# Optimization experiments

Hardware: AMD Instinct MI355X
Metric: run time of the kernel (lower is better)

Reference implementation:

```python
import jax, jax.numpy as jnp
import numpy as np

N, D_IN = 8192, 256
L1_DIMS = [256, 128, 64]   # linear_list1
GNN_DIMS = [64, 64]        # gnn_list
L2_DIMS = [64, 32]         # linear_list2


def leaky(x):
    return jnp.where(x >= 0, x, 0.1 * x)


def _lin_params(key, din, dout, scale=0.05):
    k1, k2 = jax.random.split(key)
    W = jax.random.normal(k1, (dout, din), dtype=jnp.float32) * scale
    b = jax.random.normal(k2, (dout,), dtype=jnp.float32) * scale
    return W, b


def setup_inputs() -> dict:
    key = jax.random.key(0)
    ks = jax.random.split(key, 8)
    x = jax.random.normal(ks[0], (N, D_IN), dtype=jnp.float32)
    A = jax.random.uniform(ks[1], (N, N), dtype=jnp.float32)
    W1_0, b1_0 = _lin_params(ks[2], L1_DIMS[0], L1_DIMS[1])
    W1_1, b1_1 = _lin_params(ks[3], L1_DIMS[1], L1_DIMS[2])
    a = jax.random.normal(ks[4], (L1_DIMS[-1],), dtype=jnp.float32)
    Wg_0, bg_0 = _lin_params(ks[5], GNN_DIMS[0], GNN_DIMS[1])
    W2_0, b2_0 = _lin_params(ks[6], L2_DIMS[0], L2_DIMS[1])
    return {"x": x, "A": A, "W1_0": W1_0, "b1_0": b1_0, "W1_1": W1_1,
            "b1_1": b1_1, "a": a, "Wg_0": Wg_0, "bg_0": bg_0,
            "W2_0": W2_0, "b2_0": b2_0}


def reference(x, A, W1_0, b1_0, W1_1, b1_1, a, Wg_0, bg_0, W2_0, b2_0):
    # MLP encoder (linear_list1) with leakyrelu(0.1)
    x = leaky(x @ W1_0.T + b1_0)
    x = leaky(x @ W1_1.T + b1_1)  # [N, 64]

    # GAT-style scores: (x_i - x_j) @ a == s_i - s_j with s = x @ a
    s = x @ a                               # [N]
    S = jnp.exp(leaky(s[:, None] - s[None, :])) * A  # [N, N]
    S = S / jnp.sum(S, axis=-1, keepdims=True)

    # L1 = mean_ij( mean_d (x_i - x_j)^2 * S_ij )
    D = x.shape[-1]
    sq = jnp.sum(x * x, axis=-1) / D        # [N]
    pair_mse = sq[:, None] + sq[None, :] - (2.0 / D) * (x @ x.T)  # [N, N]
    L1 = jnp.mean(pair_mse * S)
    L2 = jnp.mean(S * S)

    # GNN layer(s): x = leakyrelu(Linear(S @ x))
    x = leaky((S @ x) @ Wg_0.T + bg_0)

    # output head (linear_list2), no activation
    x = x @ W2_0.T + b2_0
    return (x, L1, L2)
```

## Files before the change

kernel.cpp:

```cpp
#include <hip/hip_runtime.h>
#include <cstddef>

#define NROWS 8192
#define RA_STR 72

typedef __attribute__((ext_vector_type(8))) short bf16x8;
typedef __attribute__((ext_vector_type(4))) short short4v;
typedef __attribute__((ext_vector_type(4))) float f32x4;

__device__ __forceinline__ short f2bf(float f) {
  unsigned u = __float_as_uint(f);
  u += 0x7fffu + ((u >> 16) & 1u);
  return (short)(u >> 16);
}
__device__ __forceinline__ float leaky_f(float v) { return v >= 0.0f ? v : 0.1f * v; }

extern "C" __global__ void __launch_bounds__(256)
encoder_kernel(const float* __restrict__ x, const float* __restrict__ W10,
               const float* __restrict__ b10, const float* __restrict__ W11,
               const float* __restrict__ b11, const float* __restrict__ avec,
               float* __restrict__ x2, float* __restrict__ sarr,
               float* __restrict__ sqarr, short* __restrict__ x2bfT) {
  __shared__ float xr[4][256];
  __shared__ float h1[4][128];
  const int t = threadIdx.x;
  const int r0 = blockIdx.x * 4;
#pragma unroll
  for (int r = 0; r < 4; ++r) xr[r][t] = x[(size_t)(r0 + r) * 256 + t];
  __syncthreads();
  if (t < 128) {
    float acc[4];
    const float b = b10[t];
#pragma unroll
    for (int r = 0; r < 4; ++r) acc[r] = b;
    const float* wrow = W10 + t * 256;
    for (int c = 0; c < 256; c += 4) {
      const float4 wv = *(const float4*)(wrow + c);
#pragma unroll
      for (int r = 0; r < 4; ++r) {
        acc[r] = fmaf(wv.x, xr[r][c], acc[r]);
        acc[r] = fmaf(wv.y, xr[r][c + 1], acc[r]);
        acc[r] = fmaf(wv.z, xr[r][c + 2], acc[r]);
        acc[r] = fmaf(wv.w, xr[r][c + 3], acc[r]);
      }
    }
#pragma unroll
    for (int r = 0; r < 4; ++r) h1[r][t] = leaky_f(acc[r]);
  }
  __syncthreads();
  if (t < 64) {
    float acc[4];
    const float b = b11[t];
#pragma unroll
    for (int r = 0; r < 4; ++r) acc[r] = b;
    const float* wrow = W11 + t * 128;
    for (int c = 0; c < 128; c += 4) {
      const float4 wv = *(const float4*)(wrow + c);
#pragma unroll
      for (int r = 0; r < 4; ++r) {
        acc[r] = fmaf(wv.x, h1[r][c], acc[r]);
        acc[r] = fmaf(wv.y, h1[r][c + 1], acc[r]);
        acc[r] = fmaf(wv.z, h1[r][c + 2], acc[r]);
        acc[r] = fmaf(wv.w, h1[r][c + 3], acc[r]);
      }
    }
    const float av = avec[t];
#pragma unroll
    for (int r = 0; r < 4; ++r) {
      const float v = leaky_f(acc[r]);
      x2[(size_t)(r0 + r) * 64 + t] = v;
      x2bfT[(size_t)t * NROWS + r0 + r] = f2bf(v);
      float ps = v * av, pq = v * v;
#pragma unroll
      for (int off = 1; off < 64; off <<= 1) {
        ps += __shfl_xor(ps, off);
        pq += __shfl_xor(pq, off);
      }
      if (t == 0) { sarr[r0 + r] = ps; sqarr[r0 + r] = pq * (1.0f / 64.0f); }
    }
  }
}

extern "C" __global__ void __launch_bounds__(256)
fused_attn_kernel(const float* __restrict__ A, const float* __restrict__ sarr,
                  const float* __restrict__ sqarr, const short* __restrict__ x2bfT,
                  float* __restrict__ yp, float* __restrict__ rsp,
                  float* __restrict__ ssp, float* __restrict__ wsp) {
  __shared__ short rawA[64 * RA_STR];
  __shared__ short xbT[64 * RA_STR];
  __shared__ float sj[64];
  __shared__ float sqj[64];

  const int t = threadIdx.x;
  const int bi = blockIdx.x & 127;
  const int js = blockIdx.x >> 7;
  const int i0 = bi * 64;
  const int jbase = js * 2048;
  const int lane = t & 63;
  const int w = t >> 6;

  const int lrb = t >> 4;
  const int lc = (t & 15) * 4;

  float si[4];
#pragma unroll
  for (int p = 0; p < 4; ++p) si[p] = sarr[i0 + lrb + 16 * p];

  float prsum[4] = {0.f, 0.f, 0.f, 0.f};
  float psumsq[4] = {0.f, 0.f, 0.f, 0.f};
  float pwsq[4] = {0.f, 0.f, 0.f, 0.f};

  const int m0 = (w >> 1) * 32;
  const int n0 = (w & 1) * 32;
  const int fr = lane & 15;
  const int fk = (lane >> 4) * 8;

  f32x4 acc[2][2];
#pragma unroll
  for (int fm = 0; fm < 2; ++fm)
#pragma unroll
    for (int fn = 0; fn < 2; ++fn)
      acc[fm][fn] = (f32x4){0.f, 0.f, 0.f, 0.f};

  float4 areg[4];
#pragma unroll
  for (int p = 0; p < 4; ++p)
    areg[p] = *(const float4*)(A + (size_t)(i0 + lrb + 16 * p) * NROWS + jbase + lc);

  for (int tile = 0; tile < 32; ++tile) {
    const int j0 = jbase + tile * 64;
    __syncthreads();
    if (t < 64) { sj[t] = sarr[j0 + t]; sqj[t] = sqarr[j0 + t]; }
#pragma unroll
    for (int p = 0; p < 4; ++p) {
      const int d = lrb + 16 * p;
      const short4v v = *(const short4v*)(x2bfT + (size_t)d * NROWS + j0 + lc);
      *(short4v*)(xbT + d * RA_STR + lc) = v;
    }
    __syncthreads();
#pragma unroll
    for (int p = 0; p < 4; ++p) {
      const float s_i = si[p];
      const float4 av = areg[p];
      const float r0v = __expf(leaky_f(s_i - sj[lc + 0])) * av.x;
      const float r1v = __expf(leaky_f(s_i - sj[lc + 1])) * av.y;
      const float r2v = __expf(leaky_f(s_i - sj[lc + 2])) * av.z;
      const float r3v = __expf(leaky_f(s_i - sj[lc + 3])) * av.w;
      prsum[p] += (r0v + r1v) + (r2v + r3v);
      psumsq[p] += (r0v * r0v + r1v * r1v) + (r2v * r2v + r3v * r3v);
      pwsq[p] += r0v * sqj[lc + 0] + r1v * sqj[lc + 1] + r2v * sqj[lc + 2] + r3v * sqj[lc + 3];
      short4v bw;
      bw[0] = f2bf(r0v); bw[1] = f2bf(r1v); bw[2] = f2bf(r2v); bw[3] = f2bf(r3v);
      *(short4v*)(rawA + (lrb + 16 * p) * RA_STR + lc) = bw;
    }
    {
      const int jn = jbase + ((tile + 1) & 31) * 64;
#pragma unroll
      for (int p = 0; p < 4; ++p)
        areg[p] = *(const float4*)(A + (size_t)(i0 + lrb + 16 * p) * NROWS + jn + lc);
    }
    __syncthreads();
#pragma unroll
    for (int ks = 0; ks < 2; ++ks) {
      const bf16x8 af0 = *(const bf16x8*)(rawA + (m0 + fr) * RA_STR + ks * 32 + fk);
      const bf16x8 af1 = *(const bf16x8*)(rawA + (m0 + 16 + fr) * RA_STR + ks * 32 + fk);
      const bf16x8 bv0 = *(const bf16x8*)(xbT + (n0 + fr) * RA_STR + ks * 32 + fk);
      const bf16x8 bv1 = *(const bf16x8*)(xbT + (n0 + 16 + fr) * RA_STR + ks * 32 + fk);
      acc[0][0] = __builtin_amdgcn_mfma_f32_16x16x32_bf16(af0, bv0, acc[0][0], 0, 0, 0);
      acc[0][1] = __builtin_amdgcn_mfma_f32_16x16x32_bf16(af0, bv1, acc[0][1], 0, 0, 0);
      acc[1][0] = __builtin_amdgcn_mfma_f32_16x16x32_bf16(af1, bv0, acc[1][0], 0, 0, 0);
      acc[1][1] = __builtin_amdgcn_mfma_f32_16x16x32_bf16(af1, bv1, acc[1][1], 0, 0, 0);
    }
  }

#pragma unroll
  for (int p = 0; p < 4; ++p) {
#pragma unroll
    for (int off = 1; off < 16; off <<= 1) {
      prsum[p] += __shfl_xor(prsum[p], off);
      psumsq[p] += __shfl_xor(psumsq[p], off);
      pwsq[p] += __shfl_xor(pwsq[p], off);
    }
  }
  if ((t & 15) == 0) {
#pragma unroll
    for (int p = 0; p < 4; ++p) {
      const int gi = i0 + lrb + 16 * p;
      rsp[js * NROWS + gi] = prsum[p];
      ssp[js * NROWS + gi] = psumsq[p];
      wsp[js * NROWS + gi] = pwsq[p];
    }
  }

  float* ypb = yp + (size_t)js * NROWS * 64;
#pragma unroll
  for (int fm = 0; fm < 2; ++fm)
#pragma unroll
    for (int fn = 0; fn < 2; ++fn)
#pragma unroll
      for (int ri = 0; ri < 4; ++ri) {
        const int row = i0 + m0 + fm * 16 + ((lane >> 4) << 2) + ri;
        const int col = n0 + fn * 16 + (lane & 15);
        ypb[(size_t)row * 64 + col] = acc[fm][fn][ri];
      }
}

extern "C" __global__ void __launch_bounds__(256)
finish_kernel(const float* __restrict__ x2, const float* __restrict__ sqarr,
              const float* __restrict__ yp, const float* __restrict__ rsp,
              const float* __restrict__ ssp, const float* __restrict__ wsp,
              const float* __restrict__ Wg, const float* __restrict__ bg,
              const float* __restrict__ W2, const float* __restrict__ b2,
              float* __restrict__ outp, float* __restrict__ l1c, float* __restrict__ l2c) {
  __shared__ float hbuf[4][64];
  __shared__ float gbuf[4][64];
  const int t = threadIdx.x;
  const int w = t >> 6, lane = t & 63;
  const int i = blockIdx.x * 4 + w;

  float yv = 0.f, rowsum = 0.f, sumsq = 0.f, wsq = 0.f;
#pragma unroll
  for (int p = 0; p < 4; ++p) {
    yv += yp[(size_t)p * NROWS * 64 + (size_t)i * 64 + lane];
    rowsum += rsp[p * NROWS + i];
    sumsq += ssp[p * NROWS + i];
    wsq += wsp[p * NROWS + i];
  }
  const float inv = 1.0f / rowsum;
  hbuf[w][lane] = yv * inv;
  const float xv = x2[(size_t)i * 64 + lane];
  float xy = xv * yv;
#pragma unroll
  for (int off = 1; off < 64; off <<= 1) xy += __shfl_xor(xy, off);
  if (lane == 0) {
    l1c[i] = sqarr[i] + (wsq - (2.0f / 64.0f) * xy) * inv;
    l2c[i] = sumsq * inv * inv;
  }
  __syncthreads();
  float accg = bg[lane];
  {
    const float* wrow = Wg + lane * 64;
#pragma unroll 4
    for (int d = 0; d < 64; ++d) accg = fmaf(wrow[d], hbuf[w][d], accg);
  }
  gbuf[w][lane] = leaky_f(accg);
  __syncthreads();
  if (lane < 32) {
    float acco = b2[lane];
    const float* wrow = W2 + lane * 64;
#pragma unroll 4
    for (int d = 0; d < 64; ++d) acco = fmaf(wrow[d], gbuf[w][d], acco);
    outp[(size_t)i * 32 + lane] = acco;
  }
}

extern "C" __global__ void __launch_bounds__(256)
loss_kernel(const float* __restrict__ l1c, const float* __restrict__ l2c,
            float* __restrict__ outp) {
  __shared__ float s1[256], s2[256];
  const int t = threadIdx.x;
  float a1 = 0.f, a2 = 0.f;
  for (int i = t; i < NROWS; i += 256) { a1 += l1c[i]; a2 += l2c[i]; }
  s1[t] = a1; s2[t] = a2;
  __syncthreads();
  for (int off = 128; off > 0; off >>= 1) {
    if (t < off) { s1[t] += s1[t + off]; s2[t] += s2[t + off]; }
    __syncthreads();
  }
  if (t == 0) {
    const float scale = 1.0f / ((float)NROWS * (float)NROWS);
    outp[NROWS * 32] = s1[0] * scale;
    outp[NROWS * 32 + 1] = s2[0] * scale;
  }
}

extern "C" void kernel_launch(void* const* d_in, const int* in_sizes, int n_in,
                              void* d_out, int out_size, void* d_ws, size_t ws_size,
                              hipStream_t stream) {
  const float* x   = (const float*)d_in[0];
  const float* A   = (const float*)d_in[1];
  const float* W10 = (const float*)d_in[2];
  const float* b10 = (const float*)d_in[3];
  const float* W11 = (const float*)d_in[4];
  const float* b11 = (const float*)d_in[5];
  const float* av  = (const float*)d_in[6];
  const float* Wg  = (const float*)d_in[7];
  const float* bg  = (const float*)d_in[8];
  const float* W2  = (const float*)d_in[9];
  const float* b2  = (const float*)d_in[10];
  float* out = (float*)d_out;

  float* ws    = (float*)d_ws;
  float* x2    = ws;
  float* sarr  = x2 + (size_t)NROWS * 64;
  float* sqarr = sarr + NROWS;
  float* yp    = sqarr + NROWS;
  float* rsp   = yp + (size_t)4 * NROWS * 64;
  float* ssp   = rsp + 4 * NROWS;
  float* wsp   = ssp + 4 * NROWS;
  float* l1c   = wsp + 4 * NROWS;
  float* l2c   = l1c + NROWS;
  short* x2bfT = (short*)(l2c + NROWS);

  hipLaunchKernelGGL(encoder_kernel, dim3(2048), dim3(256), 0, stream,
                     x, W10, b10, W11, b11, av, x2, sarr, sqarr, x2bfT);
  hipLaunchKernelGGL(fused_attn_kernel, dim3(512), dim3(256), 0, stream,
                     A, sarr, sqarr, x2bfT, yp, rsp, ssp, wsp);
  hipLaunchKernelGGL(finish_kernel, dim3(2048), dim3(256), 0, stream,
                     x2, sqarr, yp, rsp, ssp, wsp, Wg, bg, W2, b2, out, l1c, l2c);
  hipLaunchKernelGGL(loss_kernel, dim3(1), dim3(256), 0, stream, l1c, l2c, out);
}
```

Measured before the change: 180.6 us.

## Load A and x2 fragments directly into MFMA registers, drop LDS staging, widen j-split

The attention kernel now has each lane compute exp-weighted A values directly in the MFMA A-operand layout and load x2bfT B fragments straight from global memory. This removes the per-tile LDS round-trips and three __syncthreads per tile. Each wave owns 16 rows and all 64 output columns, and the next A tile is prefetched with double-buffered registers. The launcher also raises the j-split to 8 when workspace allows, doubling the grid for more parallelism at the cost of larger partial buffers and more reduction work in finish_kernel. B fragments are now read uncoalesced from global memory, relying on cache hits.

```diff
diff --git a/kernel.cpp b/kernel.cpp
--- a/kernel.cpp
+++ b/kernel.cpp
@@ -2,10 +2,8 @@
 #include <cstddef>
 
 #define NROWS 8192
-#define RA_STR 72
 
 typedef __attribute__((ext_vector_type(8))) short bf16x8;
-typedef __attribute__((ext_vector_type(4))) short short4v;
 typedef __attribute__((ext_vector_type(4))) float f32x4;
 
 __device__ __forceinline__ short f2bf(float f) {
@@ -81,128 +79,130 @@
   }
 }
 
+
+__device__ __forceinline__ void do_tile(int tt, int ntiles,
+    const float* __restrict__ Ap, const short* __restrict__ Bp,
+    const float* __restrict__ sjb, const float* __restrict__ sqb,
+    float si, float4 (&cur)[4], float4 (&nxt)[4],
+    f32x4 (&acc)[4], float& prs, float& pss, float& pws) {
+  const int off = tt * 64;
+  bf16x8 bfr[2][4];
+#pragma unroll
+  for (int ks = 0; ks < 2; ++ks)
+#pragma unroll
+    for (int n = 0; n < 4; ++n)
+      bfr[ks][n] = *(const bf16x8*)(Bp + (size_t)n * 16 * NROWS + off + ks * 32);
+  const int pt = (tt + 1 == ntiles) ? 0 : tt + 1;
+#pragma unroll
+  for (int ks = 0; ks < 2; ++ks) {
+    nxt[ks * 2]     = *(const float4*)(Ap + pt * 64 + ks * 32);
+    nxt[ks * 2 + 1] = *(const float4*)(Ap + pt * 64 + ks * 32 + 4);
+  }
+  bf16x8 araw[2];
+#pragma unroll
+  for (int ks = 0; ks < 2; ++ks) {
+    const float4 sl = *(const float4*)(sjb + off + ks * 32);
+    const float4 sh = *(const float4*)(sjb + off + ks * 32 + 4);
+    const float4 ql = *(const float4*)(sqb + off + ks * 32);
+    const float4 qh = *(const float4*)(sqb + off + ks * 32 + 4);
+    const float4 al = cur[ks * 2];
+    const float4 ah = cur[ks * 2 + 1];
+    const float r0 = __expf(leaky_f(si - sl.x)) * al.x;
+    const float r1 = __expf(leaky_f(si - sl.y)) * al.y;
+    const float r2 = __expf(leaky_f(si - sl.z)) * al.z;
+    const float r3 = __expf(leaky_f(si - sl.w)) * al.w;
+    const float r4 = __expf(leaky_f(si - sh.x)) * ah.x;
+    const float r5 = __expf(leaky_f(si - sh.y)) * ah.y;
+    const float r6 = __expf(leaky_f(si - sh.z)) * ah.z;
+    const float r7 = __expf(leaky_f(si - sh.w)) * ah.w;
+    prs += ((r0 + r1) + (r2 + r3)) + ((r4 + r5) + (r6 + r7));
+    pss = fmaf(r0, r0, pss); pss = fmaf(r1, r1, pss);
+    pss = fmaf(r2, r2, pss); pss = fmaf(r3, r3, pss);
+    pss = fmaf(r4, r4, pss); pss = fmaf(r5, r5, pss);
+    pss = fmaf(r6, r6, pss); pss = fmaf(r7, r7, pss);
+    pws = fmaf(r0, ql.x, pws); pws = fmaf(r1, ql.y, pws);
+    pws = fmaf(r2, ql.z, pws); pws = fmaf(r3, ql.w, pws);
+    pws = fmaf(r4, qh.x, pws); pws = fmaf(r5, qh.y, pws);
+    pws = fmaf(r6, qh.z, pws); pws = fmaf(r7, qh.w, pws);
+    bf16x8 p;
+    p[0] = f2bf(r0); p[1] = f2bf(r1); p[2] = f2bf(r2); p[3] = f2bf(r3);
+    p[4] = f2bf(r4); p[5] = f2bf(r5); p[6] = f2bf(r6); p[7] = f2bf(r7);
+    araw[ks] = p;
+  }
+#pragma unroll
+  for (int ks = 0; ks < 2; ++ks)
+#pragma unroll
+    for (int n = 0; n < 4; ++n)
+      acc[n] = __builtin_amdgcn_mfma_f32_16x16x32_bf16(araw[ks], bfr[ks][n], acc[n], 0, 0, 0);
+}
+
 extern "C" __global__ void __launch_bounds__(256)
 fused_attn_kernel(const float* __restrict__ A, const float* __restrict__ sarr,
                   const float* __restrict__ sqarr, const short* __restrict__ x2bfT,
                   float* __restrict__ yp, float* __restrict__ rsp,
-                  float* __restrict__ ssp, float* __restrict__ wsp) {
-  __shared__ short rawA[64 * RA_STR];
-  __shared__ short xbT[64 * RA_STR];
-  __shared__ float sj[64];
-  __shared__ float sqj[64];
-
+                  float* __restrict__ ssp, float* __restrict__ wsp,
+                  int jspan) {
+  __shared__ float sjbuf[2048];
+  __shared__ float sqbuf[2048];
   const int t = threadIdx.x;
   const int bi = blockIdx.x & 127;
   const int js = blockIdx.x >> 7;
   const int i0 = bi * 64;
-  const int jbase = js * 2048;
+  const int jbase = js * jspan;
   const int lane = t & 63;
   const int w = t >> 6;
-
-  const int lrb = t >> 4;
-  const int lc = (t & 15) * 4;
-
-  float si[4];
-#pragma unroll
-  for (int p = 0; p < 4; ++p) si[p] = sarr[i0 + lrb + 16 * p];
-
-  float prsum[4] = {0.f, 0.f, 0.f, 0.f};
-  float psumsq[4] = {0.f, 0.f, 0.f, 0.f};
-  float pwsq[4] = {0.f, 0.f, 0.f, 0.f};
-
-  const int m0 = (w >> 1) * 32;
-  const int n0 = (w & 1) * 32;
   const int fr = lane & 15;
-  const int fk = (lane >> 4) * 8;
-
-  f32x4 acc[2][2];
-#pragma unroll
-  for (int fm = 0; fm < 2; ++fm)
-#pragma unroll
-    for (int fn = 0; fn < 2; ++fn)
-      acc[fm][fn] = (f32x4){0.f, 0.f, 0.f, 0.f};
-
-  float4 areg[4];
-#pragma unroll
-  for (int p = 0; p < 4; ++p)
-    areg[p] = *(const float4*)(A + (size_t)(i0 + lrb + 16 * p) * NROWS + jbase + lc);
-
-  for (int tile = 0; tile < 32; ++tile) {
-    const int j0 = jbase + tile * 64;
-    __syncthreads();
-    if (t < 64) { sj[t] = sarr[j0 + t]; sqj[t] = sqarr[j0 + t]; }
-#pragma unroll
-    for (int p = 0; p < 4; ++p) {
-      const int d = lrb + 16 * p;
-      const short4v v = *(const short4v*)(x2bfT + (size_t)d * NROWS + j0 + lc);
-      *(short4v*)(xbT + d * RA_STR + lc) = v;
-    }
-    __syncthreads();
-#pragma unroll
-    for (int p = 0; p < 4; ++p) {
-      const float s_i = si[p];
-      const float4 av = areg[p];
-      const float r0v = __expf(leaky_f(s_i - sj[lc + 0])) * av.x;
-      const float r1v = __expf(leaky_f(s_i - sj[lc + 1])) * av.y;
-      const float r2v = __expf(leaky_f(s_i - sj[lc + 2])) * av.z;
-      const float r3v = __expf(leaky_f(s_i - sj[lc + 3])) * av.w;
-      prsum[p] += (r0v + r1v) + (r2v + r3v);
-      psumsq[p] += (r0v * r0v + r1v * r1v) + (r2v * r2v + r3v * r3v);
-      pwsq[p] += r0v * sqj[lc + 0] + r1v * sqj[lc + 1] + r2v * sqj[lc + 2] + r3v * sqj[lc + 3];
-      short4v bw;
-      bw[0] = f2bf(r0v); bw[1] = f2bf(r1v); bw[2] = f2bf(r2v); bw[3] = f2bf(r3v);
-      *(short4v*)(rawA + (lrb + 16 * p) * RA_STR + lc) = bw;
-    }
-    {
-      const int jn = jbase + ((tile + 1) & 31) * 64;
-#pragma unroll
-      for (int p = 0; p < 4; ++p)
-        areg[p] = *(const float4*)(A + (size_t)(i0 + lrb + 16 * p) * NROWS + jn + lc);
-    }
-    __syncthreads();
-#pragma unroll
-    for (int ks = 0; ks < 2; ++ks) {
-      const bf16x8 af0 = *(const bf16x8*)(rawA + (m0 + fr) * RA_STR + ks * 32 + fk);
-      const bf16x8 af1 = *(const bf16x8*)(rawA + (m0 + 16 + fr) * RA_STR + ks * 32 + fk);
-      const bf16x8 bv0 = *(const bf16x8*)(xbT + (n0 + fr) * RA_STR + ks * 32 + fk);
-      const bf16x8 bv1 = *(const bf16x8*)(xbT + (n0 + 16 + fr) * RA_STR + ks * 32 + fk);
-      acc[0][0] = __builtin_amdgcn_mfma_f32_16x16x32_bf16(af0, bv0, acc[0][0], 0, 0, 0);
-      acc[0][1] = __builtin_amdgcn_mfma_f32_16x16x32_bf16(af0, bv1, acc[0][1], 0, 0, 0);
-      acc[1][0] = __builtin_amdgcn_mfma_f32_16x16x32_bf16(af1, bv0, acc[1][0], 0, 0, 0);
-      acc[1][1] = __builtin_amdgcn_mfma_f32_16x16x32_bf16(af1, bv1, acc[1][1], 0, 0, 0);
-    }
-  }
-
-#pragma unroll
-  for (int p = 0; p < 4; ++p) {
-#pragma unroll
-    for (int off = 1; off < 16; off <<= 1) {
-      prsum[p] += __shfl_xor(prsum[p], off);
-      psumsq[p] += __shfl_xor(psumsq[p], off);
-      pwsq[p] += __shfl_xor(pwsq[p], off);
-    }
-  }
-  if ((t & 15) == 0) {
-#pragma unroll
-    for (int p = 0; p < 4; ++p) {
-      const int gi = i0 + lrb + 16 * p;
-      rsp[js * NROWS + gi] = prsum[p];
-      ssp[js * NROWS + gi] = psumsq[p];
-      wsp[js * NROWS + gi] = pwsq[p];
-    }
-  }
-
+  const int kg = lane >> 4;
+  const int ntiles = jspan >> 6;
+
+  for (int k = t; k < jspan; k += 256) {
+    sjbuf[k] = sarr[jbase + k];
+    sqbuf[k] = sqarr[jbase + k];
+  }
+  const int irow = i0 + w * 16 + fr;
+  const float si = sarr[irow];
+  __syncthreads();
+
+  const float* Ap  = A + (size_t)irow * NROWS + jbase + kg * 8;
+  const short* Bp  = x2bfT + (size_t)fr * NROWS + jbase + kg * 8;
+  const float* sjb = sjbuf + kg * 8;
+  const float* sqb = sqbuf + kg * 8;
+
+  f32x4 acc[4];
+#pragma unroll
+  for (int n = 0; n < 4; ++n) acc[n] = (f32x4){0.f, 0.f, 0.f, 0.f};
+  float prs = 0.f, pss = 0.f, pws = 0.f;
+
+  float4 aA[4], aB[4];
+#pragma unroll
+  for (int ks = 0; ks < 2; ++ks) {
+    aA[ks * 2]     = *(const float4*)(Ap + ks * 32);
+    aA[ks * 2 + 1] = *(const float4*)(Ap + ks * 32 + 4);
+  }
+
+  for (int tt = 0; tt < ntiles; tt += 2) {
+    do_tile(tt,     ntiles, Ap, Bp, sjb, sqb, si, aA, aB, acc, prs, pss, pws);
+    do_tile(tt + 1, ntiles, Ap, Bp, sjb, sqb, si, aB, aA, acc, prs, pss, pws);
+  }
+
+#pragma unroll
+  for (int off = 16; off < 64; off <<= 1) {
+    prs += __shfl_xor(prs, off);
+    pss += __shfl_xor(pss, off);
+    pws += __shfl_xor(pws, off);
+  }
+  if (lane < 16) {
+    const int gi = i0 + w * 16 + lane;
+    rsp[js * NROWS + gi] = prs;
+    ssp[js * NROWS + gi] = pss;
+    wsp[js * NROWS + gi] = pws;
+  }
   float* ypb = yp + (size_t)js * NROWS * 64;
 #pragma unroll
-  for (int fm = 0; fm < 2; ++fm)
-#pragma unroll
-    for (int fn = 0; fn < 2; ++fn)
-#pragma unroll
-      for (int ri = 0; ri < 4; ++ri) {
-        const int row = i0 + m0 + fm * 16 + ((lane >> 4) << 2) + ri;
-        const int col = n0 + fn * 16 + (lane & 15);
-        ypb[(size_t)row * 64 + col] = acc[fm][fn][ri];
-      }
+  for (int n = 0; n < 4; ++n)
+#pragma unroll
+    for (int ri = 0; ri < 4; ++ri)
+      ypb[(size_t)(i0 + w * 16 + kg * 4 + ri) * 64 + n * 16 + fr] = acc[n][ri];
 }
 
 extern "C" __global__ void __launch_bounds__(256)
@@ -211,7 +211,8 @@
               const float* __restrict__ ssp, const float* __restrict__ wsp,
               const float* __restrict__ Wg, const float* __restrict__ bg,
               const float* __restrict__ W2, const float* __restrict__ b2,
-              float* __restrict__ outp, float* __restrict__ l1c, float* __restrict__ l2c) {
+              float* __restrict__ outp, float* __restrict__ l1c, float* __restrict__ l2c,
+              int jsplit) {
   __shared__ float hbuf[4][64];
   __shared__ float gbuf[4][64];
   const int t = threadIdx.x;
@@ -219,8 +220,7 @@
   const int i = blockIdx.x * 4 + w;
 
   float yv = 0.f, rowsum = 0.f, sumsq = 0.f, wsq = 0.f;
-#pragma unroll
-  for (int p = 0; p < 4; ++p) {
+  for (int p = 0; p < jsplit; ++p) {
     yv += yp[(size_t)p * NROWS * 64 + (size_t)i * 64 + lane];
     rowsum += rsp[p * NROWS + i];
     sumsq += ssp[p * NROWS + i];
@@ -290,23 +290,31 @@
   const float* b2  = (const float*)d_in[10];
   float* out = (float*)d_out;
 
+  const size_t fixed_floats = (size_t)NROWS * 64 + 4 * (size_t)NROWS;
+  auto need = [&](int js) {
+    return (fixed_floats + (size_t)js * NROWS * 64 + 3 * (size_t)js * NROWS) * 4
+           + (size_t)NROWS * 64 * 2;
+  };
+  int jsplit = (ws_size >= need(8)) ? 8 : 4;
+  const int jspan = NROWS / jsplit;
+
   float* ws    = (float*)d_ws;
   float* x2    = ws;
   float* sarr  = x2 + (size_t)NROWS * 64;
   float* sqarr = sarr + NROWS;
   float* yp    = sqarr + NROWS;
-  float* rsp   = yp + (size_t)4 * NROWS * 64;
-  float* ssp   = rsp + 4 * NROWS;
-  float* wsp   = ssp + 4 * NROWS;
-  float* l1c   = wsp + 4 * NROWS;
+  float* rsp   = yp + (size_t)jsplit * NROWS * 64;
+  float* ssp   = rsp + (size_t)jsplit * NROWS;
+  float* wsp   = ssp + (size_t)jsplit * NROWS;
+  float* l1c   = wsp + (size_t)jsplit * NROWS;
   float* l2c   = l1c + NROWS;
   short* x2bfT = (short*)(l2c + NROWS);
 
   hipLaunchKernelGGL(encoder_kernel, dim3(2048), dim3(256), 0, stream,
                      x, W10, b10, W11, b11, av, x2, sarr, sqarr, x2bfT);
-  hipLaunchKernelGGL(fused_attn_kernel, dim3(512), dim3(256), 0, stream,
-                     A, sarr, sqarr, x2bfT, yp, rsp, ssp, wsp);
+  hipLaunchKernelGGL(fused_attn_kernel, dim3(128 * jsplit), dim3(256), 0, stream,
+                     A, sarr, sqarr, x2bfT, yp, rsp, ssp, wsp, jspan);
   hipLaunchKernelGGL(finish_kernel, dim3(2048), dim3(256), 0, stream,
-                     x2, sqarr, yp, rsp, ssp, wsp, Wg, bg, W2, b2, out, l1c, l2c);
+                     x2, sqarr, yp, rsp, ssp, wsp, Wg, bg, W2, b2, out, l1c, l2c, jsplit);
   hipLaunchKernelGGL(loss_kernel, dim3(1), dim3(256), 0, stream, l1c, l2c, out);
 }
```

Result: slower. 268.2 us (+48.5%).
